# Performance work log

Measured on AMD Instinct MI355X. Metric: run time of the kernel, lower is better.

The kernel has to match this reference:

```python
import jax, jax.numpy as jnp
import numpy as np

KH, KW = 3, 3
IN_CH, OUT_CH = 16, 128
H, W_IN = 64, 64
HO, WO = H - KH + 1, W_IN - KW + 1  # 62, 62


def setup_inputs() -> dict:
    key = jax.random.key(0)
    kx, kw = jax.random.split(key)
    x = jax.random.normal(kx, (16, IN_CH, H, W_IN), dtype=jnp.float32)
    W = jax.random.normal(kw, (OUT_CH, IN_CH * (KH * KW) ** 2), dtype=jnp.float32)
    return {"x": x, "W": W}


def _unfold(x):
    # torch nn.Unfold ordering: (B, C*kh*kw, L) with channel-major, then kernel
    # positions row-major. Build (B, L, C, kd) to match transpose(1,2).view(...).
    B = x.shape[0]
    patches = jnp.stack(
        [x[:, :, i:i + HO, j:j + WO] for i in range(KH) for j in range(KW)],
        axis=2,
    )  # (B, C, kd, HO, WO)
    # -> (B, L, C, kd)
    return patches.reshape(B, IN_CH, KH * KW, HO * WO).transpose(0, 3, 1, 2)


def reference(x, W):
    B = x.shape[0]
    p = _unfold(x)  # (B, L, C, kd)
    # per-patch, per-channel self outer product: (B, L, C, kd, kd)
    outer = jnp.einsum("blci,blcj->blcij", p, p)
    feat = outer.reshape(B, HO * WO, -1)  # (B, L, C*kd*kd)
    out = jnp.einsum("blf,of->bol", feat, W)  # (B, O, L)
    # fold with (1,1) kernel == reshape to spatial grid
    return out.reshape(B, OUT_CH, HO, WO)
```

## Files before the change

### kernel.cpp

```cpp
#include <hip/hip_runtime.h>
#include <hip/hip_bf16.h>

#define BATCH 16
#define INCH 16
#define HH 64
#define WW 64
#define HO 62
#define WO 62
#define LTOT (HO * WO)
#define OUTCH 128
#define KFULL 1296
#define NTRI 45
#define NSC 8
#define KPC 96
#define TILE_N 124
#define NTILES 31
#define FROW 52
#define NFRAG (2 * NSC * 3 * 4 * 64)

typedef short bf16x8 __attribute__((ext_vector_type(8)));
typedef float f32x4 __attribute__((ext_vector_type(4)));

__device__ constexpr int TRI_A[NTRI] = {
  0,0,0,0,0,0,0,0,0, 1,1,1,1,1,1,1,1, 2,2,2,2,2,2,2,
  3,3,3,3,3,3, 4,4,4,4,4, 5,5,5,5, 6,6,6, 7,7, 8};
__device__ constexpr int TRI_B[NTRI] = {
  0,1,2,3,4,5,6,7,8, 1,2,3,4,5,6,7,8, 2,3,4,5,6,7,8,
  3,4,5,6,7,8, 4,5,6,7,8, 5,6,7,8, 6,7,8, 7,8, 8};

__device__ inline unsigned short f2bf(float x) {
  unsigned int u = __float_as_uint(x);
  unsigned int r = ((u >> 16) & 1u) + 0x7FFFu;
  return (unsigned short)((u + r) >> 16);
}
__device__ inline unsigned int pack2(float lo, float hi) {
  __hip_bfloat162 h = __float22bfloat162_rn(make_float2(lo, hi));
  return *reinterpret_cast<unsigned int*>(&h);
}

__device__ inline float wsym_at(const float* __restrict__ W, int sc, int o, int kl) {
  int half = kl >= 48 ? 1 : 0;
  int t = kl - 48 * half;
  if (t >= NTRI) return 0.f;
  int a = TRI_A[t], b = TRI_B[t];
  int c = sc * 2 + half;
  float v = W[o * KFULL + c * 81 + a * 9 + b];
  if (a != b) v += W[o * KFULL + c * 81 + b * 9 + a];
  return v;
}

__global__ void prep_wfrag(const float* __restrict__ W, unsigned short* __restrict__ Wf) {
  int idx = blockIdx.x * 256 + threadIdx.x;
  if (idx >= NFRAG) return;
  int lane = idx & 63;
  int mf = (idx >> 6) & 3;
  int rest = idx >> 8;
  int kc = rest % 3;
  int scg = rest / 3;
  int sc = scg & 7, g = scg >> 3;
  int o = g * 64 + mf * 16 + (lane & 15);
  int k0 = kc * 32 + (lane >> 4) * 8;
  unsigned short v[8];
#pragma unroll
  for (int e = 0; e < 8; ++e) v[e] = f2bf(wsym_at(W, sc, o, k0 + e));
  uint4 pk;
  pk.x = (unsigned)v[0] | ((unsigned)v[1] << 16);
  pk.y = (unsigned)v[2] | ((unsigned)v[3] << 16);
  pk.z = (unsigned)v[4] | ((unsigned)v[5] << 16);
  pk.w = (unsigned)v[6] | ((unsigned)v[7] << 16);
  *(uint4*)&Wf[(size_t)idx * 8] = pk;
}

template <bool USE_WS>
__global__ __launch_bounds__(256, 2) void conv2o_ping(
    const float* __restrict__ X, const float* __restrict__ Wraw,
    const uint4* __restrict__ Wf, float* __restrict__ Out) {
  __shared__ float xs[INCH][4][64];
  __shared__ unsigned int Fl[2][128 * FROW];

  const int tid = threadIdx.x;
  const int blk = blockIdx.x;
  const int b = blk / NTILES;
  const int tile = blk % NTILES;
  const int y0 = tile * 2;
  const int l0 = tile * TILE_N;

  const int lane = tid & 63;
  const int wave = tid >> 6;
  const int g = wave >> 1;
  const int mbase = g * 64;
  const int nbase = (wave & 1) * 64;
  const int lr = lane & 15;
  const int lh = lane >> 4;

#pragma unroll
  for (int t = 0; t < 4; ++t) {
    int i = tid + t * 256;
    int chr = i >> 4, seg = i & 15;
    int ch = chr >> 2, r = chr & 3;
    *(float4*)&xs[ch][r][seg * 4] =
        *(const float4*)&X[((size_t)(b * INCH + ch) * HH + (y0 + r)) * WW + seg * 4];
  }

  const int q = tid & 127;
  const int half = tid >> 7;
  const int qrow = q / 62;
  const int qcol = q - qrow * 62;

  auto computeF = [&](int scn, int buf) {
    const unsigned base = q * FROW + half * 24;
    if (q < TILE_N) {
      const int ch = scn * 2 + half;
      float p[9];
#pragma unroll
      for (int di = 0; di < 3; ++di)
#pragma unroll
        for (int dj = 0; dj < 3; ++dj)
          p[di * 3 + dj] = xs[ch][qrow + di][qcol + dj];
#pragma unroll
      for (int j = 0; j < 6; ++j) {
        unsigned int d[4];
#pragma unroll
        for (int w = 0; w < 4; ++w) {
          const int m = 4 * j + w;
          float lo = (2 * m < NTRI) ? p[TRI_A[2 * m]] * p[TRI_B[2 * m]] : 0.f;
          float hi = (2 * m + 1 < NTRI) ? p[TRI_A[2 * m + 1]] * p[TRI_B[2 * m + 1]] : 0.f;
          d[w] = pack2(lo, hi);
        }
        *(uint4*)&Fl[buf][base + j * 4] = make_uint4(d[0], d[1], d[2], d[3]);
      }
    } else {
      const uint4 z = make_uint4(0u, 0u, 0u, 0u);
#pragma unroll
      for (int j = 0; j < 6; ++j) *(uint4*)&Fl[buf][base + j * 4] = z;
    }
  };

  auto loadA = [&](uint4* ap, int sc) {
    if (USE_WS) {
      const uint4* basep = Wf + (size_t)((g * NSC + sc) * 3) * 4 * 64;
#pragma unroll
      for (int f = 0; f < 12; ++f) ap[f] = basep[f * 64 + lane];
    } else {
#pragma unroll
      for (int kc = 0; kc < 3; ++kc)
#pragma unroll
        for (int mf = 0; mf < 4; ++mf) {
          const int o = mbase + mf * 16 + lr;
          const int k0 = kc * 32 + lh * 8;
          unsigned short v[8];
#pragma unroll
          for (int e = 0; e < 8; ++e) v[e] = f2bf(wsym_at(Wraw, sc, o, k0 + e));
          uint4 pk;
          pk.x = (unsigned)v[0] | ((unsigned)v[1] << 16);
          pk.y = (unsigned)v[2] | ((unsigned)v[3] << 16);
          pk.z = (unsigned)v[4] | ((unsigned)v[5] << 16);
          pk.w = (unsigned)v[6] | ((unsigned)v[7] << 16);
          ap[kc * 4 + mf] = pk;
        }
    }
  };

  f32x4 acc[4][4];
#pragma unroll
  for (int mf = 0; mf < 4; ++mf)
#pragma unroll
    for (int nf = 0; nf < 4; ++nf) acc[mf][nf] = (f32x4){0.f, 0.f, 0.f, 0.f};

  auto mfmaStep = [&](const uint4* ap, int buf) {
#pragma unroll
    for (int kc = 0; kc < 3; ++kc) {
      const int koff = kc * 16 + lh * 4;
      bf16x8 bfr[4];
#pragma unroll
      for (int nf = 0; nf < 4; ++nf)
        bfr[nf] = *(const bf16x8*)&Fl[buf][(nbase + nf * 16 + lr) * FROW + koff];
#pragma unroll
      for (int mf = 0; mf < 4; ++mf) {
        const bf16x8 af = __builtin_bit_cast(bf16x8, ap[kc * 4 + mf]);
#pragma unroll
        for (int nf = 0; nf < 4; ++nf)
          acc[mf][nf] = __builtin_amdgcn_mfma_f32_16x16x32_bf16(af, bfr[nf], acc[mf][nf], 0, 0, 0);
      }
    }
  };

  __syncthreads();

  uint4 apfA[12], apfB[12];
  loadA(apfA, 0);
  computeF(0, 0);
  __syncthreads();

#pragma unroll 1
  for (int it = 0; it < 4; ++it) {
    const int sc = 2 * it;
    loadA(apfB, sc + 1);
    computeF(sc + 1, 1);
    mfmaStep(apfA, 0);
    __syncthreads();
    if (it < 3) {
      loadA(apfA, sc + 2);
      computeF(sc + 2, 0);
    }
    mfmaStep(apfB, 1);
    __syncthreads();
  }

#pragma unroll
  for (int nf = 0; nf < 4; ++nf) {
    const int pos = nbase + nf * 16 + lr;
    if (pos < TILE_N) {
      const int l = l0 + pos;
#pragma unroll
      for (int mf = 0; mf < 4; ++mf) {
        const int o = mbase + mf * 16 + lh * 4;
        float* outp = &Out[((size_t)(b * OUTCH + o)) * LTOT + l];
#pragma unroll
        for (int r = 0; r < 4; ++r) outp[(size_t)r * LTOT] = acc[mf][nf][r];
      }
    }
  }
}

extern "C" void kernel_launch(void* const* d_in, const int* in_sizes, int n_in,
                              void* d_out, int out_size, void* d_ws, size_t ws_size,
                              hipStream_t stream) {
  const float* X = (const float*)d_in[0];
  const float* W = (const float*)d_in[1];
  float* Out = (float*)d_out;

  const size_t wf_bytes = (size_t)NFRAG * 16;
  const int use_ws = (ws_size >= wf_bytes) ? 1 : 0;

  if (use_ws) {
    prep_wfrag<<<(NFRAG + 255) / 256, 256, 0, stream>>>(W, (unsigned short*)d_ws);
    conv2o_ping<true><<<BATCH * NTILES, 256, 0, stream>>>(X, W, (const uint4*)d_ws, Out);
  } else {
    conv2o_ping<false><<<BATCH * NTILES, 256, 0, stream>>>(X, W, (const uint4*)d_ws, Out);
  }
}
```

Before: 87.03 us.

## Tile one output row per 128-thread block and XOR-swizzle feature LDS

```diff
diff --git a/kernel.cpp b/kernel.cpp
--- a/kernel.cpp
+++ b/kernel.cpp
@@ -12,9 +12,7 @@
 #define KFULL 1296
 #define NTRI 45
 #define NSC 8
-#define KPC 96
-#define TILE_N 124
-#define NTILES 31
+#define TILE 62
 #define FROW 52
 #define NFRAG (2 * NSC * 3 * 4 * 64)
 
@@ -72,51 +70,48 @@
 }
 
 template <bool USE_WS>
-__global__ __launch_bounds__(256, 2) void conv2o_ping(
+__global__ __launch_bounds__(128, 2) void conv2o_row(
     const float* __restrict__ X, const float* __restrict__ Wraw,
     const uint4* __restrict__ Wf, float* __restrict__ Out) {
-  __shared__ float xs[INCH][4][64];
-  __shared__ unsigned int Fl[2][128 * FROW];
+  __shared__ float xs[INCH][3][64];
+  __shared__ unsigned int Fl[2][64 * FROW];
 
   const int tid = threadIdx.x;
   const int blk = blockIdx.x;
-  const int b = blk / NTILES;
-  const int tile = blk % NTILES;
-  const int y0 = tile * 2;
-  const int l0 = tile * TILE_N;
+  const int b = blk / HO;
+  const int y = blk % HO;
+  const int l0 = y * WO;
 
   const int lane = tid & 63;
-  const int wave = tid >> 6;
-  const int g = wave >> 1;
+  const int g = tid >> 6;
   const int mbase = g * 64;
-  const int nbase = (wave & 1) * 64;
   const int lr = lane & 15;
   const int lh = lane >> 4;
 
 #pragma unroll
-  for (int t = 0; t < 4; ++t) {
-    int i = tid + t * 256;
-    int chr = i >> 4, seg = i & 15;
-    int ch = chr >> 2, r = chr & 3;
+  for (int t = 0; t < 6; ++t) {
+    int i = tid + t * 128;
+    int ch = i / 48;
+    int rem = i % 48;
+    int r = rem / 16, seg = rem % 16;
     *(float4*)&xs[ch][r][seg * 4] =
-        *(const float4*)&X[((size_t)(b * INCH + ch) * HH + (y0 + r)) * WW + seg * 4];
-  }
-
-  const int q = tid & 127;
-  const int half = tid >> 7;
-  const int qrow = q / 62;
-  const int qcol = q - qrow * 62;
+        *(const float4*)&X[((size_t)(b * INCH + ch) * HH + (y + r)) * WW + seg * 4];
+  }
+
+  const int q = tid & 63;
+  const int half = tid >> 6;
+  const int xorw = ((q >> 3) & 3) << 2;
 
   auto computeF = [&](int scn, int buf) {
-    const unsigned base = q * FROW + half * 24;
-    if (q < TILE_N) {
+    const unsigned base = (unsigned)q * FROW;
+    if (q < TILE) {
       const int ch = scn * 2 + half;
       float p[9];
 #pragma unroll
       for (int di = 0; di < 3; ++di)
 #pragma unroll
         for (int dj = 0; dj < 3; ++dj)
-          p[di * 3 + dj] = xs[ch][qrow + di][qcol + dj];
+          p[di * 3 + dj] = xs[ch][di][q + dj];
 #pragma unroll
       for (int j = 0; j < 6; ++j) {
         unsigned int d[4];
@@ -127,12 +122,16 @@
           float hi = (2 * m + 1 < NTRI) ? p[TRI_A[2 * m + 1]] * p[TRI_B[2 * m + 1]] : 0.f;
           d[w] = pack2(lo, hi);
         }
-        *(uint4*)&Fl[buf][base + j * 4] = make_uint4(d[0], d[1], d[2], d[3]);
+        const int col = (half * 24 + j * 4) ^ xorw;
+        *(uint4*)&Fl[buf][base + col] = make_uint4(d[0], d[1], d[2], d[3]);
       }
     } else {
       const uint4 z = make_uint4(0u, 0u, 0u, 0u);
 #pragma unroll
-      for (int j = 0; j < 6; ++j) *(uint4*)&Fl[buf][base + j * 4] = z;
+      for (int j = 0; j < 6; ++j) {
+        const int col = (half * 24 + j * 4) ^ xorw;
+        *(uint4*)&Fl[buf][base + col] = z;
+      }
     }
   };
 
@@ -173,8 +172,11 @@
       const int koff = kc * 16 + lh * 4;
       bf16x8 bfr[4];
 #pragma unroll
-      for (int nf = 0; nf < 4; ++nf)
-        bfr[nf] = *(const bf16x8*)&Fl[buf][(nbase + nf * 16 + lr) * FROW + koff];
+      for (int nf = 0; nf < 4; ++nf) {
+        const int row = nf * 16 + lr;
+        const int col = koff ^ (((row >> 3) & 3) << 2);
+        bfr[nf] = *(const bf16x8*)&Fl[buf][row * FROW + col];
+      }
 #pragma unroll
       for (int mf = 0; mf < 4; ++mf) {
         const bf16x8 af = __builtin_bit_cast(bf16x8, ap[kc * 4 + mf]);
@@ -185,10 +187,9 @@
     }
   };
 
-  __syncthreads();
-
   uint4 apfA[12], apfB[12];
   loadA(apfA, 0);
+  __syncthreads();
   computeF(0, 0);
   __syncthreads();
 
@@ -209,8 +210,8 @@
 
 #pragma unroll
   for (int nf = 0; nf < 4; ++nf) {
-    const int pos = nbase + nf * 16 + lr;
-    if (pos < TILE_N) {
+    const int pos = nf * 16 + lr;
+    if (pos < TILE) {
       const int l = l0 + pos;
 #pragma unroll
       for (int mf = 0; mf < 4; ++mf) {
@@ -235,8 +236,8 @@
 
   if (use_ws) {
     prep_wfrag<<<(NFRAG + 255) / 256, 256, 0, stream>>>(W, (unsigned short*)d_ws);
-    conv2o_ping<true><<<BATCH * NTILES, 256, 0, stream>>>(X, W, (const uint4*)d_ws, Out);
+    conv2o_row<true><<<BATCH * HO, 128, 0, stream>>>(X, W, (const uint4*)d_ws, Out);
   } else {
-    conv2o_ping<false><<<BATCH * NTILES, 256, 0, stream>>>(X, W, (const uint4*)d_ws, Out);
-  }
-}
+    conv2o_row<false><<<BATCH * HO, 128, 0, stream>>>(X, W, (const uint4*)d_ws, Out);
+  }
+}
```

Result: no change. 86.58 us (-0.5%).
